# Optimization experiments

Measured on AMD Instinct MI355X. Metric: run time of the kernel, lower is better.

## Reference

```python
import jax, jax.numpy as jnp
import numpy as np

N, L, HH, WW, E, NH = 8, 300, 96, 96, 256, 8


def setup_inputs() -> dict:
    key = jax.random.key(0)
    ks = jax.random.split(key, 9)
    return {
        "query_row": jax.random.normal(ks[0], (N, L, E), dtype=jnp.float32),
        "query_col": jax.random.normal(ks[1], (N, L, E), dtype=jnp.float32),
        "key_row": jax.random.normal(ks[2], (N, HH, WW, E), dtype=jnp.float32),
        "key_col": jax.random.normal(ks[3], (N, HH, WW, E), dtype=jnp.float32),
        "value": jax.random.normal(ks[4], (N, HH, WW, E), dtype=jnp.float32),
        "in_proj_weight": jax.random.normal(ks[5], (5 * E, E), dtype=jnp.float32) * 0.02,
        "in_proj_bias": jax.random.normal(ks[6], (5 * E,), dtype=jnp.float32) * 0.02,
        "out_proj_weight": jax.random.normal(ks[7], (E, E), dtype=jnp.float32) * 0.02,
        "out_proj_bias": jax.random.normal(ks[8], (E,), dtype=jnp.float32) * 0.02,
        "num_heads": NH,
    }


def reference(query_row, query_col, key_row, key_col, value,
              in_proj_weight, in_proj_bias, out_proj_weight, out_proj_bias,
              num_heads):
    bsz, tgt_len, embed_dim = query_row.shape
    head_dim = embed_dim // num_heads
    scaling = float(head_dim) ** -0.5

    def proj(x, i):
        w = in_proj_weight[i * embed_dim:(i + 1) * embed_dim]
        b = in_proj_bias[i * embed_dim:(i + 1) * embed_dim]
        return x @ w.T + b

    q_row = proj(query_row, 0) * scaling          # (N, L, E)
    q_col = proj(query_col, 1) * scaling          # (N, L, E)
    k_row = proj(key_row, 2).mean(axis=1)         # mean over H -> (N, W, E)
    k_col = proj(key_col, 3).mean(axis=2)         # mean over W -> (N, H, E)
    v = proj(value, 4)                            # (N, H, W, E)

    heads = lambda t: t.reshape(*t.shape[:-1], num_heads, head_dim)
    qr, qc, kr, kc = heads(q_row), heads(q_col), heads(k_row), heads(k_col)
    vh = heads(v)                                 # (N, H, W, nh, hd)

    # additive row/col decomposed scores -> independent softmaxes
    w_row = jax.nn.softmax(jnp.einsum('blnd,bwnd->bnlw', qr, kr), axis=-1)  # (N,nh,L,W)
    w_col = jax.nn.softmax(jnp.einsum('blnd,bhnd->bnlh', qc, kc), axis=-1)  # (N,nh,L,H)

    # contract col weights with value over H, then row weights over W
    tmp = jnp.einsum('bnlh,bhwnd->bnlwd', w_col, vh)       # (N,nh,L,W,hd)
    out = jnp.einsum('bnlw,bnlwd->blnd', w_row, tmp)       # (N,L,nh,hd)
    out = out.reshape(bsz, tgt_len, embed_dim).transpose(1, 0, 2)  # (L,N,E)
    return out @ out_proj_weight.T + out_proj_bias
```

## Files before the change

### kernel.cpp

```cpp
#include <hip/hip_runtime.h>
#include <cstdint>


typedef __attribute__((ext_vector_type(8))) short short8v;
typedef __attribute__((ext_vector_type(4))) short short4v;
typedef __attribute__((ext_vector_type(4))) float f32x4;

#define SCALE_Q 0.17677669529663687f

#define GLL16(gp, lp)                                                   \
  __builtin_amdgcn_global_load_lds(                                     \
      (const __attribute__((address_space(1))) void*)(gp),              \
      (__attribute__((address_space(3))) void*)(lp), 16, 0, 0)

__device__ __forceinline__ unsigned short f2bf(float x) {
  unsigned int u = __builtin_bit_cast(unsigned int, x);
  u += 0x7FFFu + ((u >> 16) & 1u);
  return (unsigned short)(u >> 16);
}

__device__ __forceinline__ unsigned int cvtpk(float a, float b) {
  unsigned int r;
  asm("v_cvt_pk_bf16_f32 %0, %1, %2" : "=v"(r) : "v"(a), "v"(b));
  return r;
}

__device__ __forceinline__ short8v pack8cvt(const f32x4& lo, const f32x4& hi) {
  union { short8v s; unsigned int u[4]; } z;
  z.u[0] = cvtpk(lo[0], lo[1]);
  z.u[1] = cvtpk(lo[2], lo[3]);
  z.u[2] = cvtpk(hi[0], hi[1]);
  z.u[3] = cvtpk(hi[2], hi[3]);
  return z.s;
}

__device__ __forceinline__ short4v pack4cvt(float a, float b, float c, float d) {
  union { short4v s; unsigned int u[2]; } z;
  z.u[0] = cvtpk(a, b);
  z.u[1] = cvtpk(c, d);
  return z.s;
}

__device__ __forceinline__ short8v pack8(const float4& fa, const float4& fb) {
  short8v v;
  v[0] = (short)f2bf(fa.x); v[1] = (short)f2bf(fa.y);
  v[2] = (short)f2bf(fa.z); v[3] = (short)f2bf(fa.w);
  v[4] = (short)f2bf(fb.x); v[5] = (short)f2bf(fb.y);
  v[6] = (short)f2bf(fb.z); v[7] = (short)f2bf(fb.w);
  return v;
}

__global__ __launch_bounds__(256) void cvt_w_kernel(const float* __restrict__ w_in,
                                                    const float* __restrict__ w_out,
                                                    short* __restrict__ Wb) {
  int idx = blockIdx.x * 256 + threadIdx.x;
  float v = (idx < 327680) ? w_in[idx] : w_out[idx - 327680];
  Wb[idx] = (short)f2bf(v);
}

__global__ __launch_bounds__(256) void mean_over_h_v3(const float* __restrict__ in,
                                                      float* __restrict__ out) {
  __shared__ float4 part[256];
  int bw = blockIdx.x;
  int b = bw / 96, w = bw - b * 96;
  int t = threadIdx.x, e4 = t & 63, hq = t >> 6;
  const float4* p = (const float4*)(in + ((size_t)b * 9216 + w) * 256) + e4 +
                    (size_t)hq * 24 * 6144;
  float4 s = {0.f, 0.f, 0.f, 0.f};
#pragma unroll
  for (int i = 0; i < 24; ++i) {
    float4 v = p[(size_t)i * 6144];
    s.x += v.x; s.y += v.y; s.z += v.z; s.w += v.w;
  }
  part[t] = s;
  __syncthreads();
  if (t < 64) {
    float4 a = part[t], c = part[t + 64], d = part[t + 128], e = part[t + 192];
    float4 o;
    o.x = (a.x + c.x + d.x + e.x) * (1.f / 96.f);
    o.y = (a.y + c.y + d.y + e.y) * (1.f / 96.f);
    o.z = (a.z + c.z + d.z + e.z) * (1.f / 96.f);
    o.w = (a.w + c.w + d.w + e.w) * (1.f / 96.f);
    ((float4*)out)[(size_t)bw * 64 + t] = o;
  }
}

__global__ __launch_bounds__(256) void mean_over_w_v3(const float* __restrict__ in,
                                                      float* __restrict__ out) {
  __shared__ float4 part[256];
  int bh = blockIdx.x;
  int t = threadIdx.x, e4 = t & 63, wq = t >> 6;
  const float4* p = (const float4*)(in + (size_t)bh * 24576) + e4 + (size_t)wq * 24 * 64;
  float4 s = {0.f, 0.f, 0.f, 0.f};
#pragma unroll
  for (int i = 0; i < 24; ++i) {
    float4 v = p[(size_t)i * 64];
    s.x += v.x; s.y += v.y; s.z += v.z; s.w += v.w;
  }
  part[t] = s;
  __syncthreads();
  if (t < 64) {
    float4 a = part[t], c = part[t + 64], d = part[t + 128], e = part[t + 192];
    float4 o;
    o.x = (a.x + c.x + d.x + e.x) * (1.f / 96.f);
    o.y = (a.y + c.y + d.y + e.y) * (1.f / 96.f);
    o.z = (a.z + c.z + d.z + e.z) * (1.f / 96.f);
    o.w = (a.w + c.w + d.w + e.w) * (1.f / 96.f);
    ((float4*)out)[(size_t)bh * 64 + t] = o;
  }
}

__global__ __launch_bounds__(256) void gemm_proj(
    const float* __restrict__ A0, const float* __restrict__ A1,
    const short* __restrict__ Wb, const float* __restrict__ bias,
    float* __restrict__ Cf, short* __restrict__ Cb0, short* __restrict__ Cb1,
    float scale, int mode) {
  __shared__ short As[32 * 264];
  int y = blockIdx.y;
  const float* A = y ? A1 : A0;
  short* Cb = y ? Cb1 : Cb0;
  const short* Wp = Wb + y * 65536;
  const float* bp = bias + y * 256;
  int t = threadIdx.x;
  int m0 = blockIdx.x * 32;
  int wave = t >> 6, lane = t & 63, r = lane & 15, g = lane >> 4;

  {
    int row = t >> 3, c0 = (t & 7) * 32;
    const float* ap = A + ((size_t)m0 + row) * 256 + c0;
    float4 ld[8];
#pragma unroll
    for (int j = 0; j < 8; ++j) ld[j] = *(const float4*)(ap + j * 4);
    short* dst = &As[row * 264 + c0];
#pragma unroll
    for (int j = 0; j < 4; ++j)
      *(short8v*)(dst + j * 8) = pack8(ld[2 * j], ld[2 * j + 1]);
  }
  __syncthreads();

  f32x4 acc[2][4] = {};
  const short* wbase = Wp + (size_t)(wave * 64 + r) * 256;
#pragma unroll
  for (int ks = 0; ks < 8; ++ks) {
    short8v af0 = *(const short8v*)&As[r * 264 + ks * 32 + g * 8];
    short8v af1 = *(const short8v*)&As[(16 + r) * 264 + ks * 32 + g * 8];
    short8v bf[4];
#pragma unroll
    for (int nf = 0; nf < 4; ++nf)
      bf[nf] = *(const short8v*)(wbase + nf * 16 * 256 + ks * 32 + g * 8);
#pragma unroll
    for (int nf = 0; nf < 4; ++nf) {
      acc[0][nf] = __builtin_amdgcn_mfma_f32_16x16x32_bf16(af0, bf[nf], acc[0][nf], 0, 0, 0);
      acc[1][nf] = __builtin_amdgcn_mfma_f32_16x16x32_bf16(af1, bf[nf], acc[1][nf], 0, 0, 0);
    }
  }

#pragma unroll
  for (int mf = 0; mf < 2; ++mf)
#pragma unroll
    for (int nf = 0; nf < 4; ++nf) {
      int nn = wave * 64 + nf * 16 + r;
      float bval = bp[nn];
#pragma unroll
      for (int i = 0; i < 4; ++i) {
        int m = m0 + mf * 16 + g * 4 + i;
        float val = (acc[mf][nf][i] + bval) * scale;
        if (mode == 1) {
          int bb = m / 300, ll = m - bb * 300;
          Cf[((size_t)ll * 8 + bb) * 256 + nn] = val;
        } else {
          Cb[(size_t)m * 256 + nn] = (short)f2bf(val);
        }
      }
    }
}

__global__ __launch_bounds__(512, 1) void vproj_kernel(
    const float* __restrict__ A, const short* __restrict__ Wb,
    const float* __restrict__ bias, short* __restrict__ vvT) {
  __shared__ float buf[2][16 * 260];
  __shared__ short Ts[8][32 * 68];
  int t = threadIdx.x;
  int wave = t >> 6, lane = t & 63, r = lane & 15, g = lane >> 4;
  int m0g = blockIdx.x * 288;
  int b_ = blockIdx.x >> 5;
  int hw00 = (blockIdx.x & 31) * 288;
  int chbase = wave * 32;

  short8v bf[8][2];
  {
    const short* wbase = Wb + (size_t)(chbase + r) * 256;
#pragma unroll
    for (int ks = 0; ks < 8; ++ks)
#pragma unroll
      for (int nf = 0; nf < 2; ++nf)
        bf[ks][nf] = *(const short8v*)(wbase + nf * 16 * 256 + ks * 32 + g * 8);
  }
#pragma unroll
  for (int ks = 0; ks < 8; ++ks)
#pragma unroll
    for (int nf = 0; nf < 2; ++nf)
      asm volatile("" : "+a"(bf[ks][nf]));
  float bias_v[2];
#pragma unroll
  for (int nf = 0; nf < 2; ++nf) bias_v[nf] = bias[chbase + nf * 16 + r];

#pragma unroll
  for (int q = 0; q < 2; ++q) {
#pragma unroll
    for (int i = 0; i < 2; ++i) {
      int row = wave * 2 + i;
      const float* gp = A + ((size_t)m0g + q * 16 + row) * 256 + lane * 4;
      GLL16(gp, &buf[q][row * 260]);
    }
  }

  int chg = chbase + (lane & 31);
  int half = lane >> 5;
  short* vbase = vvT + (size_t)(b_ * 8 + (chg >> 5)) * 294912 +
                 (size_t)(chg & 31) * 9216 + hw00;
  const short* tsr = &Ts[wave][(lane & 31) * 68];

#pragma unroll
  for (int tt = 0; tt < 18; ++tt) {
    if (tt == 17)                 asm volatile("s_waitcnt vmcnt(0)" ::: "memory");
    else if (tt && (tt & 3) == 0) asm volatile("s_waitcnt vmcnt(6)" ::: "memory");
    else                          asm volatile("s_waitcnt vmcnt(2)" ::: "memory");
    __builtin_amdgcn_s_barrier();

    f32x4 acc[2] = {};
    const float* bp_ = &buf[tt & 1][0];
#pragma unroll
    for (int ks = 0; ks < 8; ++ks) {
      const float* p = bp_ + r * 260 + ks * 32 + g * 8;
      f32x4 lo = *(const f32x4*)p;
      f32x4 hi = *(const f32x4*)(p + 4);
      short8v af = pack8cvt(lo, hi);
      acc[0] = __builtin_amdgcn_mfma_f32_16x16x32_bf16(af, bf[ks][0], acc[0], 0, 0, 0);
      acc[1] = __builtin_amdgcn_mfma_f32_16x16x32_bf16(af, bf[ks][1], acc[1], 0, 0, 0);
    }

#pragma unroll
    for (int nf = 0; nf < 2; ++nf) {
      float bv = bias_v[nf];
      *(short4v*)&Ts[wave][(nf * 16 + r) * 68 + (tt & 3) * 16 + g * 4] =
          pack4cvt(acc[nf][0] + bv, acc[nf][1] + bv, acc[nf][2] + bv, acc[nf][3] + bv);
    }
    asm volatile("" ::: "memory");

    if ((tt & 3) == 3) {
      short* gdst = vbase + (tt >> 2) * 64 + half * 32;
      const short* src = tsr + half * 32;
#pragma unroll
      for (int j = 0; j < 4; ++j)
        *(short8v*)(gdst + j * 8) = *(const short8v*)(src + j * 8);
      asm volatile("" ::: "memory");
    } else if (tt == 17) {
      short* gdst = vbase + 256 + half * 16;
      const short* src = tsr + half * 16;
#pragma unroll
      for (int j = 0; j < 2; ++j)
        *(short8v*)(gdst + j * 8) = *(const short8v*)(src + j * 8);
      asm volatile("" ::: "memory");
    }

    __builtin_amdgcn_s_barrier();
    if (tt + 2 < 18) {
#pragma unroll
      for (int i = 0; i < 2; ++i) {
        int row = wave * 2 + i;
        const float* gp = A + ((size_t)m0g + (tt + 2) * 16 + row) * 256 + lane * 4;
        GLL16(gp, &buf[tt & 1][row * 260]);
      }
    }
  }
}

__global__ __launch_bounds__(64) void scores_softmax_v2(
    const short* __restrict__ qrb, const short* __restrict__ qcb,
    const short* __restrict__ krb, const short* __restrict__ kcb,
    short* __restrict__ wrowB, float* __restrict__ wcolT) {
  int lchunk = blockIdx.x, bn = blockIdx.y, kind = blockIdx.z;
  int b = bn >> 3, n = bn & 7;
  int lane = threadIdx.x;
  int r = lane & 15, g = lane >> 4;
  const short* qb = kind ? qcb : qrb;
  const short* kb = kind ? kcb : krb;
  int l0 = lchunk * 80;

  short8v a[5], bfr[6];
#pragma unroll
  for (int lf = 0; lf < 5; ++lf) {
    int l = l0 + lf * 16 + r;
    if (l > 299) l = 299;
    a[lf] = *(const short8v*)(qb + ((size_t)b * 300 + l) * 256 + n * 32 + g * 8);
  }
#pragma unroll
  for (int f = 0; f < 6; ++f)
    bfr[f] = *(const short8v*)(kb + ((size_t)b * 96 + f * 16 + r) * 256 + n * 32 + g * 8);

  f32x4 c[5][6];
#pragma unroll
  for (int lf = 0; lf < 5; ++lf)
#pragma unroll
    for (int f = 0; f < 6; ++f) {
      f32x4 z = {};
      c[lf][f] = __builtin_amdgcn_mfma_f32_16x16x32_bf16(a[lf], bfr[f], z, 0, 0, 0);
    }

#pragma unroll
  for (int lf = 0; lf < 5; ++lf)
#pragma unroll
    for (int i = 0; i < 4; ++i) {
      float m = c[lf][0][i];
#pragma unroll
      for (int f = 1; f < 6; ++f) m = fmaxf(m, c[lf][f][i]);
#pragma unroll
      for (int mask = 1; mask <= 8; mask <<= 1) m = fmaxf(m, __shfl_xor(m, mask, 64));
      float e[6], s = 0.f;
#pragma unroll
      for (int f = 0; f < 6; ++f) { e[f] = __expf(c[lf][f][i] - m); s += e[f]; }
#pragma unroll
      for (int mask = 1; mask <= 8; mask <<= 1) s += __shfl_xor(s, mask, 64);
      float inv = 1.f / s;
#pragma unroll
      for (int f = 0; f < 6; ++f) c[lf][f][i] = e[f] * inv;
    }

  if (kind == 0) {
#pragma unroll
    for (int lf = 0; lf < 5; ++lf)
#pragma unroll
      for (int i = 0; i < 4; ++i) {
        int l = l0 + lf * 16 + g * 4 + i;
        bool ok = (l < 300);
#pragma unroll
        for (int f = 0; f < 6; ++f) {
          float wv = ok ? c[lf][f][i] : 0.f;
          wrowB[((size_t)bn * 320 + l) * 96 + f * 16 + r] = (short)f2bf(wv);
        }
      }
  } else {
#pragma unroll
    for (int lf = 0; lf < 5; ++lf)
#pragma unroll
      for (int f = 0; f < 6; ++f) {
        int l = l0 + lf * 16 + g * 4;
        f32x4 wv = c[lf][f];
#pragma unroll
        for (int i = 0; i < 4; ++i) if (l + i >= 300) wv[i] = 0.f;
        *(f32x4*)(wcolT + ((size_t)bn * 96 + f * 16 + r) * 320 + l) = wv;
      }
  }
}

__global__ __launch_bounds__(512) void attn_kernel(
    const short* __restrict__ wrowB, const float* __restrict__ wcolT,
    const short* __restrict__ vvT, float* __restrict__ ao) {
  __shared__ f32x4 cmb[3][2][4][64];
  int i = blockIdx.x;
  int xcd = i & 7, j = i >> 3;
  int bn = (j / 5) * 8 + xcd;
  int lh = j - (j / 5) * 5;
  int b = bn >> 3, n = bn & 7;
  int t = threadIdx.x, wave = t >> 6, lane = t & 63;
  int df = wave & 1, hh = wave >> 1;
  int lbase = lh * 64;
  int r = lane & 15, g = lane >> 4;

  short8v a[4][3];
  const short* wr = wrowB + (size_t)bn * 320 * 96;
#pragma unroll
  for (int lf = 0; lf < 4; ++lf)
#pragma unroll
    for (int ks = 0; ks < 3; ++ks)
      a[lf][ks] = *(const short8v*)(wr + (lbase + lf * 16 + r) * 96 + ks * 32 + g * 8);

  const short* vb = vvT + (size_t)bn * 294912 + (size_t)(df * 16 + r) * 9216 + hh * 24 * 96;
  const float* wcb = wcolT + ((size_t)bn * 96 + hh * 24) * 320 + lbase + g * 4;

  f32x4 acc[4] = {};
  short8v b0[3], b1[3];
  f32x4 w0[4], w1[4];
#pragma unroll
  for (int ks = 0; ks < 3; ++ks) b0[ks] = *(const short8v*)(vb + ks * 32 + g * 8);
#pragma unroll
  for (int lf = 0; lf < 4; ++lf) w0[lf] = *(const f32x4*)(wcb + lf * 16);

  for (int h2 = 0; h2 < 12; ++h2) {
    int h = h2 * 2;
#pragma unroll
    for (int ks = 0; ks < 3; ++ks) b1[ks] = *(const short8v*)(vb + (h + 1) * 96 + ks * 32 + g * 8);
#pragma unroll
    for (int lf = 0; lf < 4; ++lf) w1[lf] = *(const f32x4*)(wcb + (h + 1) * 320 + lf * 16);
    {
      f32x4 R[4] = {};
#pragma unroll
      for (int ks = 0; ks < 3; ++ks)
#pragma unroll
        for (int lf = 0; lf < 4; ++lf)
          R[lf] = __builtin_amdgcn_mfma_f32_16x16x32_bf16(a[lf][ks], b0[ks], R[lf], 0, 0, 0);
#pragma unroll
      for (int lf = 0; lf < 4; ++lf) acc[lf] += w0[lf] * R[lf];
    }
    if (h2 < 11) {
#pragma unroll
      for (int ks = 0; ks < 3; ++ks) b0[ks] = *(const short8v*)(vb + (h + 2) * 96 + ks * 32 + g * 8);
#pragma unroll
      for (int lf = 0; lf < 4; ++lf) w0[lf] = *(const f32x4*)(wcb + (h + 2) * 320 + lf * 16);
    }
    {
      f32x4 R[4] = {};
#pragma unroll
      for (int ks = 0; ks < 3; ++ks)
#pragma unroll
        for (int lf = 0; lf < 4; ++lf)
          R[lf] = __builtin_amdgcn_mfma_f32_16x16x32_bf16(a[lf][ks], b1[ks], R[lf], 0, 0, 0);
#pragma unroll
      for (int lf = 0; lf < 4; ++lf) acc[lf] += w1[lf] * R[lf];
    }
  }

  if (hh > 0) {
#pragma unroll
    for (int lf = 0; lf < 4; ++lf) cmb[hh - 1][df][lf][lane] = acc[lf];
  }
  __syncthreads();
  if (hh == 0) {
#pragma unroll
    for (int lf = 0; lf < 4; ++lf) {
      f32x4 o = acc[lf];
#pragma unroll
      for (int q = 0; q < 3; ++q) o += cmb[q][df][lf][lane];
#pragma unroll
      for (int i2 = 0; i2 < 4; ++i2) {
        int l = lbase + lf * 16 + g * 4 + i2;
        if (l < 300)
          ao[((size_t)b * 300 + l) * 256 + n * 32 + df * 16 + r] = o[i2];
      }
    }
  }
}

extern "C" void kernel_launch(void* const* d_in, const int* in_sizes, int n_in,
                              void* d_out, int out_size, void* d_ws, size_t ws_size,
                              hipStream_t stream) {
  const float* query_row = (const float*)d_in[0];
  const float* query_col = (const float*)d_in[1];
  const float* key_row   = (const float*)d_in[2];
  const float* key_col   = (const float*)d_in[3];
  const float* value     = (const float*)d_in[4];
  const float* W         = (const float*)d_in[5];
  const float* Bv        = (const float*)d_in[6];
  const float* Wout      = (const float*)d_in[7];
  const float* Bout      = (const float*)d_in[8];

  float* ws = (float*)d_ws;
  float* krm   = ws;
  float* kcm   = krm + 196608;
  float* ao    = kcm + 196608;
  float* wcolT = ao + 614400;
  short* qrb   = (short*)(wcolT + 1966080);
  short* qcb   = qrb + 614400;
  short* krb   = qcb + 614400;
  short* kcb   = krb + 196608;
  short* wrowB = kcb + 196608;
  short* vvT   = wrowB + 1966080;
  short* Wb    = vvT + 18874368;

  cvt_w_kernel<<<1536, 256, 0, stream>>>(W, Wout, Wb);
  mean_over_h_v3<<<768, 256, 0, stream>>>(key_row, krm);
  mean_over_w_v3<<<768, 256, 0, stream>>>(key_col, kcm);
  gemm_proj<<<dim3(75, 2), 256, 0, stream>>>(query_row, query_col, Wb, Bv,
                                             nullptr, qrb, qcb, SCALE_Q, 3);
  gemm_proj<<<dim3(24, 2), 256, 0, stream>>>(krm, kcm, Wb + 131072, Bv + 512,
                                             nullptr, krb, kcb, 1.f, 3);
  vproj_kernel<<<256, 512, 0, stream>>>(value, Wb + 262144, Bv + 1024, vvT);
  scores_softmax_v2<<<dim3(4, 64, 2), 64, 0, stream>>>(qrb, qcb, krb, kcb, wrowB, wcolT);
  attn_kernel<<<320, 512, 0, stream>>>(wrowB, wcolT, vvT, ao);
  gemm_proj<<<dim3(75, 1), 256, 0, stream>>>(ao, nullptr, Wb + 327680, Bout,
                                             (float*)d_out, nullptr, nullptr, 1.f, 1);
}
```

Baseline: 159.6 us.

## Split vproj and attention over more blocks, reduce attn partials in out-proj

vproj_kernel now handles 96 rows per block instead of 288 and launches 768 blocks, with a smaller transpose staging buffer and occupancy hint 4. attn_kernel splits the H reduction into two halves across 640 blocks, each writing a partial output buffer. The output projection GEMM sums the two partials while loading A. The aim is to fill more CUs on both heavy kernels, at the cost of extra partial-buffer traffic and reloading the weight fragments per block.

```diff
diff --git a/kernel.cpp b/kernel.cpp
--- a/kernel.cpp
+++ b/kernel.cpp
@@ -112,6 +112,7 @@
 
 __global__ __launch_bounds__(256) void gemm_proj(
     const float* __restrict__ A0, const float* __restrict__ A1,
+    const float* __restrict__ Aadd,
     const short* __restrict__ Wb, const float* __restrict__ bias,
     float* __restrict__ Cf, short* __restrict__ Cb0, short* __restrict__ Cb1,
     float scale, int mode) {
@@ -127,10 +128,19 @@
 
   {
     int row = t >> 3, c0 = (t & 7) * 32;
-    const float* ap = A + ((size_t)m0 + row) * 256 + c0;
+    size_t off = ((size_t)m0 + row) * 256 + c0;
+    const float* ap = A + off;
     float4 ld[8];
 #pragma unroll
     for (int j = 0; j < 8; ++j) ld[j] = *(const float4*)(ap + j * 4);
+    if (Aadd) {
+      const float* aq = Aadd + off;
+#pragma unroll
+      for (int j = 0; j < 8; ++j) {
+        float4 e = *(const float4*)(aq + j * 4);
+        ld[j].x += e.x; ld[j].y += e.y; ld[j].z += e.z; ld[j].w += e.w;
+      }
+    }
     short* dst = &As[row * 264 + c0];
 #pragma unroll
     for (int j = 0; j < 4; ++j)
@@ -175,16 +185,16 @@
     }
 }
 
-__global__ __launch_bounds__(512, 1) void vproj_kernel(
+__global__ __launch_bounds__(512, 4) void vproj_kernel(
     const float* __restrict__ A, const short* __restrict__ Wb,
     const float* __restrict__ bias, short* __restrict__ vvT) {
   __shared__ float buf[2][16 * 260];
-  __shared__ short Ts[8][32 * 68];
+  __shared__ short Ts[8][32 * 36];
   int t = threadIdx.x;
   int wave = t >> 6, lane = t & 63, r = lane & 15, g = lane >> 4;
-  int m0g = blockIdx.x * 288;
-  int b_ = blockIdx.x >> 5;
-  int hw00 = (blockIdx.x & 31) * 288;
+  int m0g = blockIdx.x * 96;
+  int b_ = blockIdx.x / 96;
+  int hw00 = (blockIdx.x - b_ * 96) * 96;
   int chbase = wave * 32;
 
   short8v bf[8][2];
@@ -219,12 +229,12 @@
   int half = lane >> 5;
   short* vbase = vvT + (size_t)(b_ * 8 + (chg >> 5)) * 294912 +
                  (size_t)(chg & 31) * 9216 + hw00;
-  const short* tsr = &Ts[wave][(lane & 31) * 68];
-
-#pragma unroll
-  for (int tt = 0; tt < 18; ++tt) {
-    if (tt == 17)                 asm volatile("s_waitcnt vmcnt(0)" ::: "memory");
-    else if (tt && (tt & 3) == 0) asm volatile("s_waitcnt vmcnt(6)" ::: "memory");
+  const short* tsr = &Ts[wave][(lane & 31) * 36];
+
+#pragma unroll
+  for (int tt = 0; tt < 6; ++tt) {
+    if (tt == 5)                  asm volatile("s_waitcnt vmcnt(0)" ::: "memory");
+    else if (tt == 2 || tt == 4)  asm volatile("s_waitcnt vmcnt(4)" ::: "memory");
     else                          asm volatile("s_waitcnt vmcnt(2)" ::: "memory");
     __builtin_amdgcn_s_barrier();
 
@@ -243,29 +253,21 @@
 #pragma unroll
     for (int nf = 0; nf < 2; ++nf) {
       float bv = bias_v[nf];
-      *(short4v*)&Ts[wave][(nf * 16 + r) * 68 + (tt & 3) * 16 + g * 4] =
+      *(short4v*)&Ts[wave][(nf * 16 + r) * 36 + (tt & 1) * 16 + g * 4] =
           pack4cvt(acc[nf][0] + bv, acc[nf][1] + bv, acc[nf][2] + bv, acc[nf][3] + bv);
     }
     asm volatile("" ::: "memory");
 
-    if ((tt & 3) == 3) {
-      short* gdst = vbase + (tt >> 2) * 64 + half * 32;
-      const short* src = tsr + half * 32;
-#pragma unroll
-      for (int j = 0; j < 4; ++j)
-        *(short8v*)(gdst + j * 8) = *(const short8v*)(src + j * 8);
+    if (tt & 1) {
+      short* gdst = vbase + (tt - 1) * 16 + half * 16;
+      const short* src = tsr + half * 16;
+      *(short8v*)gdst = *(const short8v*)src;
+      *(short8v*)(gdst + 8) = *(const short8v*)(src + 8);
       asm volatile("" ::: "memory");
-    } else if (tt == 17) {
-      short* gdst = vbase + 256 + half * 16;
-      const short* src = tsr + half * 16;
-#pragma unroll
-      for (int j = 0; j < 2; ++j)
-        *(short8v*)(gdst + j * 8) = *(const short8v*)(src + j * 8);
-      asm volatile("" ::: "memory");
     }
 
     __builtin_amdgcn_s_barrier();
-    if (tt + 2 < 18) {
+    if (tt + 2 < 6) {
 #pragma unroll
       for (int i = 0; i < 2; ++i) {
         int row = wave * 2 + i;
@@ -354,19 +356,22 @@
   }
 }
 
-__global__ __launch_bounds__(512) void attn_kernel(
+__global__ __launch_bounds__(512, 2) void attn_kernel(
     const short* __restrict__ wrowB, const float* __restrict__ wcolT,
-    const short* __restrict__ vvT, float* __restrict__ ao) {
+    const short* __restrict__ vvT, float* __restrict__ part0,
+    float* __restrict__ part1) {
   __shared__ f32x4 cmb[3][2][4][64];
   int i = blockIdx.x;
   int xcd = i & 7, j = i >> 3;
-  int bn = (j / 5) * 8 + xcd;
-  int lh = j - (j / 5) * 5;
+  int grp = j / 10, rem = j - grp * 10;
+  int bn = grp * 8 + xcd;
+  int lh = rem >> 1, hh2 = rem & 1;
   int b = bn >> 3, n = bn & 7;
   int t = threadIdx.x, wave = t >> 6, lane = t & 63;
-  int df = wave & 1, hh = wave >> 1;
+  int df = wave & 1, hq = wave >> 1;
   int lbase = lh * 64;
   int r = lane & 15, g = lane >> 4;
+  int hbase = hh2 * 48 + hq * 12;
 
   short8v a[4][3];
   const short* wr = wrowB + (size_t)bn * 320 * 96;
@@ -376,8 +381,8 @@
     for (int ks = 0; ks < 3; ++ks)
       a[lf][ks] = *(const short8v*)(wr + (lbase + lf * 16 + r) * 96 + ks * 32 + g * 8);
 
-  const short* vb = vvT + (size_t)bn * 294912 + (size_t)(df * 16 + r) * 9216 + hh * 24 * 96;
-  const float* wcb = wcolT + ((size_t)bn * 96 + hh * 24) * 320 + lbase + g * 4;
+  const short* vb = vvT + (size_t)bn * 294912 + (size_t)(df * 16 + r) * 9216 + hbase * 96;
+  const float* wcb = wcolT + ((size_t)bn * 96 + hbase) * 320 + lbase + g * 4;
 
   f32x4 acc[4] = {};
   short8v b0[3], b1[3];
@@ -387,7 +392,8 @@
 #pragma unroll
   for (int lf = 0; lf < 4; ++lf) w0[lf] = *(const f32x4*)(wcb + lf * 16);
 
-  for (int h2 = 0; h2 < 12; ++h2) {
+#pragma unroll
+  for (int h2 = 0; h2 < 6; ++h2) {
     int h = h2 * 2;
 #pragma unroll
     for (int ks = 0; ks < 3; ++ks) b1[ks] = *(const short8v*)(vb + (h + 1) * 96 + ks * 32 + g * 8);
@@ -403,7 +409,7 @@
 #pragma unroll
       for (int lf = 0; lf < 4; ++lf) acc[lf] += w0[lf] * R[lf];
     }
-    if (h2 < 11) {
+    if (h2 < 5) {
 #pragma unroll
       for (int ks = 0; ks < 3; ++ks) b0[ks] = *(const short8v*)(vb + (h + 2) * 96 + ks * 32 + g * 8);
 #pragma unroll
@@ -421,12 +427,13 @@
     }
   }
 
-  if (hh > 0) {
-#pragma unroll
-    for (int lf = 0; lf < 4; ++lf) cmb[hh - 1][df][lf][lane] = acc[lf];
+  if (hq > 0) {
+#pragma unroll
+    for (int lf = 0; lf < 4; ++lf) cmb[hq - 1][df][lf][lane] = acc[lf];
   }
   __syncthreads();
-  if (hh == 0) {
+  if (hq == 0) {
+    float* po = hh2 ? part1 : part0;
 #pragma unroll
     for (int lf = 0; lf < 4; ++lf) {
       f32x4 o = acc[lf];
@@ -436,7 +443,7 @@
       for (int i2 = 0; i2 < 4; ++i2) {
         int l = lbase + lf * 16 + g * 4 + i2;
         if (l < 300)
-          ao[((size_t)b * 300 + l) * 256 + n * 32 + df * 16 + r] = o[i2];
+          po[((size_t)b * 300 + l) * 256 + n * 32 + df * 16 + r] = o[i2];
       }
     }
   }
@@ -458,8 +465,9 @@
   float* ws = (float*)d_ws;
   float* krm   = ws;
   float* kcm   = krm + 196608;
-  float* ao    = kcm + 196608;
-  float* wcolT = ao + 614400;
+  float* part0 = kcm + 196608;
+  float* part1 = part0 + 614400;
+  float* wcolT = part1 + 614400;
   short* qrb   = (short*)(wcolT + 1966080);
   short* qcb   = qrb + 614400;
   short* krb   = qcb + 614400;
@@ -471,13 +479,13 @@
   cvt_w_kernel<<<1536, 256, 0, stream>>>(W, Wout, Wb);
   mean_over_h_v3<<<768, 256, 0, stream>>>(key_row, krm);
   mean_over_w_v3<<<768, 256, 0, stream>>>(key_col, kcm);
-  gemm_proj<<<dim3(75, 2), 256, 0, stream>>>(query_row, query_col, Wb, Bv,
+  gemm_proj<<<dim3(75, 2), 256, 0, stream>>>(query_row, query_col, nullptr, Wb, Bv,
                                              nullptr, qrb, qcb, SCALE_Q, 3);
-  gemm_proj<<<dim3(24, 2), 256, 0, stream>>>(krm, kcm, Wb + 131072, Bv + 512,
+  gemm_proj<<<dim3(24, 2), 256, 0, stream>>>(krm, kcm, nullptr, Wb + 131072, Bv + 512,
                                              nullptr, krb, kcb, 1.f, 3);
-  vproj_kernel<<<256, 512, 0, stream>>>(value, Wb + 262144, Bv + 1024, vvT);
+  vproj_kernel<<<768, 512, 0, stream>>>(value, Wb + 262144, Bv + 1024, vvT);
   scores_softmax_v2<<<dim3(4, 64, 2), 64, 0, stream>>>(qrb, qcb, krb, kcb, wrowB, wcolT);
-  attn_kernel<<<320, 512, 0, stream>>>(wrowB, wcolT, vvT, ao);
-  gemm_proj<<<dim3(75, 1), 256, 0, stream>>>(ao, nullptr, Wb + 327680, Bout,
+  attn_kernel<<<640, 512, 0, stream>>>(wrowB, wcolT, vvT, part0, part1);
+  gemm_proj<<<dim3(75, 1), 256, 0, stream>>>(part0, nullptr, part1, Wb + 327680, Bout,
                                              (float*)d_out, nullptr, nullptr, 1.f, 1);
 }
```

After: 157.7 us. No clear change (-1.2%).
